# Kernel tuning notes

Hardware: AMD Instinct MI355X
Metric: run time of the kernel (lower is better)

Reference implementation:

```python
import jax, jax.numpy as jnp
import numpy as np

T, N, C, L, H, NA, NL = 32, 64, 64, 64, 256, 16, 128


def _gru_dir(x, wi, wh, bi, bh):
    # x: [Lt, N, H] time-major; PyTorch GRU gate order (r, z, n). Returns [Lt, N, H].
    xi = jnp.einsum('tnh,gh->tng', x, wi) + bi  # precompute input projections [Lt,N,3H]
    def step(h, gi):
        gh = h @ wh.T + bh
        ir, iz, inn = jnp.split(gi, 3, -1)
        hr, hz, hn = jnp.split(gh, 3, -1)
        r = jax.nn.sigmoid(ir + hr)
        z = jax.nn.sigmoid(iz + hz)
        n = jnp.tanh(inn + r * hn)
        hnew = (1.0 - z) * n + z * h
        return hnew, hnew
    h0 = jnp.zeros((x.shape[1], wh.shape[1]), x.dtype)
    _, ys = jax.lax.scan(step, h0, xi)
    return ys


def setup_inputs() -> dict:
    key = jax.random.key(0)
    ks = jax.random.split(key, 32)
    s = 0.05
    p = {}
    p['condition'] = jax.random.normal(ks[0], (T, N, C), jnp.float32)
    p['lines'] = jax.random.randint(ks[1], (N, L), 0, NL)
    p['a_idx'] = jax.random.randint(ks[2], (T, N), 0, NA)
    p['p_idx'] = jax.random.randint(ks[3], (T, N), 0, L)
    p['embed'] = jax.random.normal(ks[4], (NL, H)) * s
    p['aemb'] = jax.random.normal(ks[5], (NA, H)) * s
    p['gru_wi_f'] = jax.random.normal(ks[6], (3 * H, H)) * s
    p['gru_wh_f'] = jax.random.normal(ks[7], (3 * H, H)) * s
    p['gru_bi_f'] = jax.random.normal(ks[8], (3 * H,)) * s
    p['gru_bh_f'] = jax.random.normal(ks[9], (3 * H,)) * s
    p['gru_wi_b'] = jax.random.normal(ks[10], (3 * H, H)) * s
    p['gru_wh_b'] = jax.random.normal(ks[11], (3 * H, H)) * s
    p['gru_bi_b'] = jax.random.normal(ks[12], (3 * H,)) * s
    p['gru_bh_b'] = jax.random.normal(ks[13], (3 * H,)) * s
    p['f_w1'] = jax.random.normal(ks[14], (H, C + H)) * s
    p['f_b1'] = jax.random.normal(ks[15], (H,)) * s
    p['f_w2'] = jax.random.normal(ks[16], (H, H)) * s
    p['f_b2'] = jax.random.normal(ks[17], (H,)) * s
    p['cell_wi'] = jax.random.normal(ks[18], (3 * H, H)) * s
    p['cell_wh'] = jax.random.normal(ks[19], (3 * H, H)) * s
    p['cell_bi'] = jax.random.normal(ks[20], (3 * H,)) * s
    p['cell_bh'] = jax.random.normal(ks[21], (3 * H,)) * s
    p['critic_w'] = jax.random.normal(ks[22], (1, H)) * s
    p['critic_b'] = jax.random.normal(ks[23], (1,)) * s
    p['pointer_w'] = jax.random.normal(ks[24], (L, H)) * s
    p['pointer_b'] = jax.random.normal(ks[25], (L,)) * s
    p['actor_w'] = jax.random.normal(ks[26], (NA, H)) * s
    p['actor_b'] = jax.random.normal(ks[27], (NA,)) * s
    p['query_w'] = jax.random.normal(ks[28], (H, H)) * s
    p['query_b'] = jax.random.normal(ks[29], (H,)) * s
    return p


def reference(condition, lines, a_idx, p_idx, embed, aemb,
              gru_wi_f, gru_wh_f, gru_bi_f, gru_bh_f,
              gru_wi_b, gru_wh_b, gru_bi_b, gru_bh_b,
              f_w1, f_b1, f_w2, f_b2,
              cell_wi, cell_wh, cell_bi, cell_bh,
              critic_w, critic_b, pointer_w, pointer_b,
              actor_w, actor_b, query_w, query_b):
    Tn, Nn = a_idx.shape
    Ln = lines.shape[1]
    Hd = embed.shape[1]
    M = embed[lines]                           # [N,L,H]
    x = jnp.transpose(M, (1, 0, 2))            # [L,N,H] time-major
    # torch.roll(x, shifts=i): rolled[i, j] = x[(j - i) % L]
    idx = (jnp.arange(Ln)[None, :] - jnp.arange(Ln)[:, None]) % Ln
    rolled = x[idx]                            # [L_roll, L_time, N, H]
    def bigru(seq):
        f = _gru_dir(seq, gru_wi_f, gru_wh_f, gru_bi_f, gru_bh_f)
        b = _gru_dir(seq[::-1], gru_wi_b, gru_wh_b, gru_bi_b, gru_bh_b)[::-1]
        return jnp.concatenate([f, b], -1)     # [L_time,N,2H]
    K1 = jax.vmap(bigru)(rolled)               # [L,L,N,2H]
    K = K1.reshape(Ln, Ln, Nn, 2, Hd).transpose(2, 0, 1, 3, 4).reshape(Nn, Ln, 2 * Ln, Hd)
    # A[t-1] for t=0 is hx.a == 0 (fresh episode, zero hidden state)
    a_prev = jnp.concatenate([jnp.zeros((1, Nn), a_idx.dtype), a_idx[:-1]], 0)
    rng_n = jnp.arange(Nn)
    def step(h, inp):
        cond_t, ap_t, p_t, a_t = inp
        obs = jnp.concatenate([cond_t, aemb[ap_t]], -1)
        xf = jax.nn.relu(obs @ f_w1.T + f_b1)
        xf = jax.nn.relu(xf @ f_w2.T + f_b2)
        gi = xf @ cell_wi.T + cell_bi
        gh = h @ cell_wh.T + cell_bh
        ir, iz, inn = jnp.split(gi, 3, -1)
        hr, hz, hn = jnp.split(gh, 3, -1)
        r = jax.nn.sigmoid(ir + hr)
        z = jax.nn.sigmoid(iz + hz)
        n = jnp.tanh(inn + r * hn)
        h = (1.0 - z) * n + z * h
        p_probs = jax.nn.softmax(h @ pointer_w.T + pointer_b, -1)
        q = h @ query_w.T + query_b
        k = K[rng_n, p_t]                      # gather: [N, 2L, H]
        l = jnp.einsum('nkh,nh->nk', k, q)
        zz = jnp.einsum('nk,nkh->nh', l, k)
        a_probs = jax.nn.softmax(zz @ actor_w.T + actor_b, -1)
        v = h @ critic_w.T + critic_b
        out = jnp.concatenate([a_t[:, None].astype(h.dtype), p_t[:, None].astype(h.dtype),
                               v, h, a_probs, p_probs], -1)
        return h, out
    h0 = jnp.zeros((Nn, Hd), condition.dtype)
    _, hxs = jax.lax.scan(step, h0, (condition, a_prev, p_idx, a_idx))
    return hxs  # packed RecurrentState: [T, N, 1+1+1+H+na+L]
```

## Files before the change

### kernel.cpp

```cpp
#include <hip/hip_runtime.h>
#include <hip/hip_bf16.h>
#include <cstddef>
#include <cstdint>

typedef __bf16 bf16;
typedef bf16 bf16x8 __attribute__((ext_vector_type(8)));
typedef float f32x4 __attribute__((ext_vector_type(4)));

#define DEV static __device__ __forceinline__

DEV f32x4 mfma_bf16(bf16x8 a, bf16x8 b, f32x4 c) {
  return __builtin_amdgcn_mfma_f32_16x16x32_bf16(a, b, c, 0, 0, 0);
}
DEV f32x4 mfma_fp8(long a, long b, f32x4 c) {
  return __builtin_amdgcn_mfma_f32_16x16x32_fp8_fp8(a, b, c, 0, 0, 0);
}

DEV float sigmoid_f(float x) { return 1.0f / (1.0f + __expf(-x)); }
DEV float tanh_f(float x) {
  float ax = fabsf(x);
  float e = __expf(-2.0f * ax);
  float t = 1.0f - 2.0f * e / (1.0f + e);
  return copysignf(t, x);
}
DEV unsigned char fp8_of(float x) {
  return (unsigned char)(__builtin_amdgcn_cvt_pk_fp8_f32(x, x, 0, false) & 0xFF);
}

static constexpr int H_ = 256;

static constexpr int o_embed = 0;
static constexpr int o_aemb = 32768;
static constexpr int o_wi_f = 36864;
static constexpr int o_wh_f = 233472;
static constexpr int o_bi_f = 430080;
static constexpr int o_bh_f = 430848;
static constexpr int o_wi_b = 431616;
static constexpr int o_wh_b = 628224;
static constexpr int o_bi_b = 824832;
static constexpr int o_bh_b = 825600;
static constexpr int o_f_w1 = 826368;
static constexpr int o_f_b1 = 908288;
static constexpr int o_f_w2 = 908544;
static constexpr int o_f_b2 = 974080;
static constexpr int o_cell_wi = 974336;
static constexpr int o_cell_wh = 1170944;
static constexpr int o_cell_bi = 1367552;
static constexpr int o_cell_bh = 1368320;
static constexpr int o_critic_w = 1369088;
static constexpr int o_critic_b = 1369344;
static constexpr int o_pointer_w = 1369360;
static constexpr int o_pointer_b = 1385744;
static constexpr int o_actor_w = 1385808;
static constexpr int o_actor_b = 1389904;
static constexpr int o_query_w = 1389920;
static constexpr int o_query_b = 1455456;
static constexpr int CW_TOTAL = 1455712;
static constexpr int WH8_TOTAL = 393216;
static constexpr int PREP_TOTAL = CW_TOTAL + WH8_TOTAL;
static constexpr int PREP_WGS = (PREP_TOTAL + 2047) / 2048;

static constexpr size_t XI_OFF = 0;
static constexpr size_t XI_BYTES = 2ull * 64 * 64 * 768 * 2;
static constexpr size_t QS_OFF = XI_OFF;
static constexpr size_t K1_OFF = XI_OFF + XI_BYTES;
static constexpr size_t K1_BYTES = 64ull * 32 * 128 * 256;
static constexpr size_t GI_OFF = K1_OFF + K1_BYTES;
static constexpr size_t GI_BYTES = 32ull * 64 * 768 * 4;
static constexpr size_t HD_OFF = GI_OFF + GI_BYTES;
static constexpr size_t HD_BYTES = 32ull * 64 * 256 * 4;
static constexpr size_t SLOT_OFF = HD_OFF + HD_BYTES;
static constexpr size_t SLOT_BYTES = 64ull * 64 * 4;
static constexpr size_t FLG_OFF = SLOT_OFF + SLOT_BYTES;
static constexpr size_t FLG_BYTES = 256;
static constexpr size_t WL_OFF = FLG_OFF + FLG_BYTES;
static constexpr size_t WL_BYTES = 8448;
static constexpr size_t CW_OFF = WL_OFF + WL_BYTES;
static constexpr size_t CW_BYTES = (size_t)CW_TOTAL * 2;
static constexpr size_t WH8_OFF = ((CW_OFF + CW_BYTES + 255) / 256) * 256;

struct PrepArgs {
  const void* src[26];
  int off[26];
  int cnt[26];
};

__global__ __launch_bounds__(256)
void k_prep(PrepArgs pa, const uint32_t* __restrict__ cond, const uint32_t* __restrict__ emb,
            const void* __restrict__ whf_src, const void* __restrict__ whb_src,
            const int* __restrict__ p_idx, int* __restrict__ flags,
            bf16* __restrict__ cw, unsigned char* __restrict__ wh8,
            int* __restrict__ slot_map, int* __restrict__ wl) {
  int bx = blockIdx.x;
  int tid = threadIdx.x;
  __shared__ int votes[256];

  int c1 = 0;
  {
    uint32_t w0 = emb[tid * 2], w1 = emb[tid * 2 + 1];
    int e0 = (int)((w0 >> 7) & 0xFF), e1 = (int)((w1 >> 7) & 0xFF);
    c1 += (e0 >= 96 && e0 <= 130) ? 1 : 0;
    c1 += (e1 >= 96 && e1 <= 130) ? 1 : 0;
  }
  votes[tid] = c1;
  __syncthreads();
  __shared__ int f32w_s;
  if (tid == 0) {
    int s = 0;
    for (int i = 0; i < 256; i++) s += votes[i];
    f32w_s = (s < 256) ? 1 : 0;
  }
  __syncthreads();
  bool f32w = f32w_s != 0;

  if (bx == 0) {
    __syncthreads();
    int c0 = 0;
    {
      uint32_t w0 = cond[tid * 2], w1 = cond[tid * 2 + 1];
      int e0 = (int)((w0 >> 7) & 0xFF), e1 = (int)((w1 >> 7) & 0xFF);
      c0 += (e0 >= 96 && e0 <= 130) ? 1 : 0;
      c0 += (e1 >= 96 && e1 <= 130) ? 1 : 0;
    }
    votes[tid] = c0;
    __syncthreads();
    if (tid == 0) {
      int s = 0;
      for (int i = 0; i < 256; i++) s += votes[i];
      flags[0] = (s < 256) ? 1 : 0;
      flags[1] = f32w ? 1 : 0;
    }
  }
// ... 5 lines not shown
      if (gidx < CW_TOTAL) {
        int rem = gidx, s = 0;
        while (s < 26 && rem >= pa.cnt[s]) { rem -= pa.cnt[s]; s++; }
        if (s < 26) {
          float v = f32w ? ((const float*)pa.src[s])[rem]
                         : (float)((const bf16*)pa.src[s])[rem];
          cw[pa.off[s] + rem] = (bf16)v;
        }
      } else {
        int i = gidx - CW_TOTAL;
        const void* src = (i < 196608) ? whf_src : whb_src;
        int k = (i < 196608) ? i : i - 196608;
        float v = f32w ? ((const float*)src)[k] : (float)((const bf16*)src)[k];
        wh8[i] = fp8_of(v);
      }
    }
    return;
  }

  __shared__ int pbuf[2048];
  __shared__ signed char sm[4096];
  __shared__ unsigned short entL[8 * 512];
  __shared__ int cntL[8];
  for (int i = tid; i < 2048; i += 256) pbuf[i] = p_idx[i];
  for (int i = tid; i < 4096; i += 256) sm[i] = -1;
  __syncthreads();
  if (tid < 64) {
    int n = tid, cnt = 0;
    for (int t = 0; t < 32; t++) {
      int p = pbuf[t * 64 + n];
      if (sm[n * 64 + p] < 0) sm[n * 64 + p] = (signed char)(cnt++);
    }
  }
  __syncthreads();
  for (int i = tid; i < 4096; i += 256) slot_map[i] = (int)sm[i];
  if (tid < 8) {
    int xcd = tid, cnt = 0;
    for (int roll = xcd * 8; roll < xcd * 8 + 8; roll++)
      for (int n = 0; n < 64; n++)
        if (sm[n * 64 + roll] >= 0) entL[xcd * 512 + (cnt++)] = (unsigned short)(n | (roll << 8));
    unsigned short pad = (unsigned short)((xcd * 8) << 8);
    while (cnt & 15) entL[xcd * 512 + (cnt++)] = pad;
    cntL[xcd] = cnt;
  }
  __syncthreads();
  if (tid < 8) wl[tid] = cntL[tid] >> 4;
  unsigned short* we = (unsigned short*)((char*)wl + 64);
  for (int i = tid; i < 8 * 512; i += 256) we[i] = entL[i];
}

__global__ __launch_bounds__(256)
void k_xi_gi(const int* __restrict__ lines, const bf16* __restrict__ cw,
             const void* __restrict__ cond_raw, const int* __restrict__ flags,
             const int* __restrict__ a_idx, bf16* __restrict__ xi,
             float* __restrict__ gi) {
  int bx = blockIdx.x;
  int tid = threadIdx.x;
  int w = tid >> 6, l = tid & 63, quad = l >> 4, l15 = l & 15;
  __shared__ __attribute__((aligned(16))) bf16 s_a[32 * 328];
  __shared__ __attribute__((aligned(16))) bf16 s_b[32 * 264];

  if (bx < 256) {
    int dir = bx & 1, rb = bx >> 1;
    const bf16* embed = cw + o_embed;
    const bf16* wi = cw + (dir ? o_wi_b : o_wi_f);
    const bf16* bi = cw + (dir ? o_bi_b : o_bi_f);
    bf16* xs = s_a;
    {
      int row = tid >> 3, seg = tid & 7;
      int grow = rb * 32 + row;
      int u = grow >> 6, n = grow & 63;
      int line = lines[n * 64 + u];
      const bf16* src = embed + (size_t)line * H_ + seg * 32;
      bf16* dst = xs + row * 264 + seg * 32;
#pragma unroll
      for (int e = 0; e < 4; e++) *(bf16x8*)(dst + e * 8) = *(const bf16x8*)(src + e * 8);
    }
    __syncthreads();
    f32x4 acc[2][12];
#pragma unroll
    for (int mt = 0; mt < 2; mt++)
#pragma unroll
      for (int nt = 0; nt < 12; nt++) acc[mt][nt] = f32x4{0.f, 0.f, 0.f, 0.f};
#pragma unroll
    for (int ks = 0; ks < 8; ks++) {
      int koff = ks * 32 + quad * 8;
      bf16x8 a0 = *(const bf16x8*)(xs + l15 * 264 + koff);
      bf16x8 a1 = *(const bf16x8*)(xs + (l15 + 16) * 264 + koff);
#pragma unroll
      for (int nt = 0; nt < 12; nt++) {
        int g = (w * 12 + nt) * 16 + l15;
        bf16x8 b = *(const bf16x8*)(wi + (size_t)g * H_ + koff);
        acc[0][nt] = mfma_bf16(a0, b, acc[0][nt]);
        acc[1][nt] = mfma_bf16(a1, b, acc[1][nt]);
      }
    }
    size_t base = (size_t)dir * 4096 * 768;
#pragma unroll
    for (int nt = 0; nt < 12; nt++) {
      int g = (w * 12 + nt) * 16 + l15;
      float bias = (float)bi[g];
#pragma unroll
      for (int mt = 0; mt < 2; mt++)
#pragma unroll
        for (int r = 0; r < 4; r++) {
          int m = mt * 16 + quad * 4 + r;
          xi[base + (size_t)(rb * 32 + m) * 768 + g] = (bf16)(acc[mt][nt][r] + bias);
        }
    }
    return;
  }

  int rb = bx - 256;
  const bf16* aemb = cw + o_aemb;
  const bf16* f_w1 = cw + o_f_w1;
  const bf16* f_b1 = cw + o_f_b1;
  const bf16* f_w2 = cw + o_f_w2;
  const bf16* f_b2 = cw + o_f_b2;
  const bf16* cell_wi = cw + o_cell_wi;
  const bf16* cell_bi = cw + o_cell_bi;
  bool cf32 = flags[0] != 0;
  bf16* obs = s_a;
  bf16* xf1 = s_b;

  for (int e = tid; e < 32 * 320; e += 256) {
    int row = e / 320, col = e - row * 320;
    int grow = rb * 32 + row;
    int t = grow >> 6, n = grow & 63;
    float v;
    if (col < 64) {
      v = cf32 ? ((const float*)cond_raw)[(size_t)grow * 64 + col]
               : (float)((const bf16*)cond_raw)[(size_t)grow * 64 + col];
    } else {
      int ap = (t == 0) ? 0 : a_idx[(t - 1) * 64 + n];
      v = (float)aemb[ap * 256 + (col - 64)];
    }
    obs[row * 328 + col] = (bf16)v;
  }
  __syncthreads();
  {
    f32x4 acc[2][4];
#pragma unroll
    for (int mt = 0; mt < 2; mt++)
#pragma unroll
      for (int nt = 0; nt < 4; nt++) acc[mt][nt] = f32x4{0.f, 0.f, 0.f, 0.f};
#pragma unroll
    for (int ks = 0; ks < 10; ks++) {
      int koff = ks * 32 + quad * 8;
      bf16x8 a0 = *(const bf16x8*)(obs + l15 * 328 + koff);
      bf16x8 a1 = *(const bf16x8*)(obs + (l15 + 16) * 328 + koff);
#pragma unroll
      for (int nt = 0; nt < 4; nt++) {
        int g = (w * 4 + nt) * 16 + l15;
        bf16x8 b = *(const bf16x8*)(f_w1 + (size_t)g * 320 + koff);
        acc[0][nt] = mfma_bf16(a0, b, acc[0][nt]);
        acc[1][nt] = mfma_bf16(a1, b, acc[1][nt]);
      }
    }
#pragma unroll
    for (int nt = 0; nt < 4; nt++) {
// ... 27 lines not shown
        bf16x8 b = *(const bf16x8*)(f_w2 + (size_t)g * 256 + koff);
        acc[0][nt] = mfma_bf16(a0, b, acc[0][nt]);
        acc[1][nt] = mfma_bf16(a1, b, acc[1][nt]);
      }
    }
#pragma unroll
    for (int nt = 0; nt < 4; nt++) {
      int g = (w * 4 + nt) * 16 + l15;
      float bias = (float)f_b2[g];
#pragma unroll
      for (int mt = 0; mt < 2; mt++)
#pragma unroll
        for (int r = 0; r < 4; r++) {
          int m = mt * 16 + quad * 4 + r;
          xf2[m * 264 + g] = (bf16)fmaxf(acc[mt][nt][r] + bias, 0.f);
        }
    }
  }
  __syncthreads();
  {
    f32x4 acc[2][12];
#pragma unroll
    for (int mt = 0; mt < 2; mt++)
#pragma unroll
      for (int nt = 0; nt < 12; nt++) acc[mt][nt] = f32x4{0.f, 0.f, 0.f, 0.f};
#pragma unroll
    for (int ks = 0; ks < 8; ks++) {
      int koff = ks * 32 + quad * 8;
      bf16x8 a0 = *(const bf16x8*)(xf2 + l15 * 264 + koff);
      bf16x8 a1 = *(const bf16x8*)(xf2 + (l15 + 16) * 264 + koff);
#pragma unroll
      for (int nt = 0; nt < 12; nt++) {
        int g = (w * 12 + nt) * 16 + l15;
        bf16x8 b = *(const bf16x8*)(cell_wi + (size_t)g * 256 + koff);
        acc[0][nt] = mfma_bf16(a0, b, acc[0][nt]);
        acc[1][nt] = mfma_bf16(a1, b, acc[1][nt]);
      }
    }
#pragma unroll
    for (int nt = 0; nt < 12; nt++) {
      int g = (w * 12 + nt) * 16 + l15;
      float bias = (float)cell_bi[g];
#pragma unroll
      for (int mt = 0; mt < 2; mt++)
#pragma unroll
        for (int r = 0; r < 4; r++) {
          int m = mt * 16 + quad * 4 + r;
          gi[(size_t)(rb * 32 + m) * 768 + g] = acc[mt][nt][r] + bias;
        }
    }
  }
}

__global__ __launch_bounds__(1024)
void k_main(const bf16* __restrict__ cw, const unsigned char* __restrict__ wh8,
            const bf16* __restrict__ xi, const int* __restrict__ slot_map,
            const int* __restrict__ wl, const float* __restrict__ gi,
            unsigned char* __restrict__ K1c, float* __restrict__ hdec) {
  int bx = blockIdx.x;
  int tid = threadIdx.x;
  int w = tid >> 6, l = tid & 63, quad = l >> 4, l15 = l & 15;
  int c = w * 16 + l15;
  __shared__ __attribute__((aligned(16))) unsigned char smem[2][16 * 264 * 2];

  if (bx < 512) {
    int xcd = bx & 7, dir = (bx >> 3) & 1, slot = bx >> 4;
    if (slot >= wl[xcd]) return;
    const unsigned short* we = (const unsigned short*)((const char*)wl + 64) + xcd * 512 + slot * 16;
    const unsigned char* whd = wh8 + (size_t)dir * 196608;
    const bf16* bh = cw + (dir ? o_bh_b : o_bh_f);

    unsigned char (*hb)[16 * 264 * 2] = smem;
    for (int idx = tid; idx < 16 * 264; idx += 1024) hb[0][idx] = 0;

    int rollv[4], nbase[4];
#pragma unroll
    for (int r = 0; r < 4; r++) {
      int e = we[quad * 4 + r];
      rollv[r] = e >> 8;
      nbase[r] = (e & 255) * 768;
    }
    int crow = tid >> 6, cseg = tid & 63;
    int ec = we[crow];
    int n_c = ec & 255, roll_c = ec >> 8;
    int kslot = slot_map[n_c * 64 + roll_c];
    unsigned char* dstb = K1c + ((size_t)n_c * 32 + (kslot < 0 ? 0 : kslot)) * 32768 + cseg * 4;

    float hreg[4] = {0.f, 0.f, 0.f, 0.f};
    float bhv[3];
    const unsigned char* bp[3];
#pragma unroll
    for (int g = 0; g < 3; g++) {
      int grow = g * 256 + c;
      bhv[g] = (float)bh[grow];
      bp[g] = whd + (size_t)grow * 256 + quad * 8;
    }
    const bf16* xid = xi + (size_t)dir * 4096 * 768;
    __syncthreads();

    int cur = 0;
    for (int t = 0; t < 64; t++) {
      int j = dir ? (63 - t) : t;
      float xiv[3][4];
#pragma unroll
      for (int r = 0; r < 4; r++) {
        int u = dir ? ((63 - t - rollv[r]) & 63) : ((t - rollv[r]) & 63);
        const bf16* xr = xid + u * 49152 + nbase[r] + c;
#pragma unroll
        for (int g = 0; g < 3; g++) xiv[g][r] = (float)xr[g * 256];
      }
      f32x4 acc[3];
#pragma unroll
      for (int g = 0; g < 3; g++) acc[g] = f32x4{0.f, 0.f, 0.f, 0.f};
#pragma unroll
      for (int ks = 0; ks < 8; ks++) {
        int ko = ks * 32 + quad * 8;
        long a0 = *(const long*)(hb[cur] + l15 * 264 + ko);
#pragma unroll
        for (int g = 0; g < 3; g++) {
          long b = *(const long*)(bp[g] + ks * 32);
          acc[g] = mfma_fp8(a0, b, acc[g]);
        }
      }
      int nxt = cur ^ 1;
#pragma unroll
      for (int r = 0; r < 4; r++) {
        float rg = sigmoid_f(xiv[0][r] + acc[0][r] + bhv[0]);
        float zg = sigmoid_f(xiv[1][r] + acc[1][r] + bhv[1]);
        float ng = tanh_f(xiv[2][r] + rg * (acc[2][r] + bhv[2]));
        hreg[r] = (1.f - zg) * ng + zg * hreg[r];
        hb[nxt][(quad * 4 + r) * 264 + c] = fp8_of(hreg[r]);
      }
      __syncthreads();
      if (kslot >= 0) {
        *(uint32_t*)(dstb + (size_t)(j * 2 + dir) * 256) =
            *(const uint32_t*)(hb[nxt] + crow * 264 + cseg * 4);
      }
      cur = nxt;
    }
    return;
  }

  int nq = bx - 512;
  const bf16* wh = cw + o_cell_wh;
  const bf16* bh = cw + o_cell_bh;
  bf16 (*hb)[16 * 264] = (bf16(*)[16 * 264])smem;
  for (int idx = tid; idx < 16 * 264; idx += 1024) hb[0][idx] = (bf16)0.f;

  float hreg[4] = {0.f, 0.f, 0.f, 0.f};
  float bhv[3];
  const bf16* bp[3];
#pragma unroll
  for (int g = 0; g < 3; g++) {
    int grow = g * 256 + c;
    bhv[g] = (float)bh[grow];
    bp[g] = wh + (size_t)grow * 256 + quad * 8;
  }
  __syncthreads();

  int cur = 0;
  for (int t = 0; t < 32; t++) {
    const float* gr = gi + ((size_t)t * 64 + nq * 16) * 768;
    float giv[3][4];
#pragma unroll
    for (int r = 0; r < 4; r++)
#pragma unroll
      for (int g = 0; g < 3; g++)
        giv[g][r] = gr[(quad * 4 + r) * 768 + g * 256 + c];

    f32x4 acc[3];
#pragma unroll
    for (int g = 0; g < 3; g++) acc[g] = f32x4{0.f, 0.f, 0.f, 0.f};
#pragma unroll
    for (int ks = 0; ks < 8; ks++) {
      int ko = ks * 32 + quad * 8;
      bf16x8 a0 = *(const bf16x8*)(hb[cur] + l15 * 264 + ko);
#pragma unroll
      for (int g = 0; g < 3; g++) {
        bf16x8 b = *(const bf16x8*)(bp[g] + ks * 32);
        acc[g] = mfma_bf16(a0, b, acc[g]);
      }
    }
    int nxt = cur ^ 1;
#pragma unroll
    for (int r = 0; r < 4; r++) {
      float rg = sigmoid_f(giv[0][r] + acc[0][r] + bhv[0]);
      float zg = sigmoid_f(giv[1][r] + acc[1][r] + bhv[1]);
      float ng = tanh_f(giv[2][r] + rg * (acc[2][r] + bhv[2]));
      float hnew = (1.f - zg) * ng + zg * hreg[r];
      hreg[r] = hnew;
      hb[nxt][(quad * 4 + r) * 264 + c] = (bf16)hnew;
      hdec[((size_t)t * 64 + nq * 16 + quad * 4 + r) * 256 + c] = hnew;
    }
    __syncthreads();
    cur = nxt;
  }
}

__global__ __launch_bounds__(256)
void k_heads(const float* __restrict__ hdec, const int* __restrict__ flags,
             const int* __restrict__ a_idx, const int* __restrict__ p_idx,
             const bf16* __restrict__ cw, float* __restrict__ qs_ws,
             void* __restrict__ out_raw) {
  int rb = blockIdx.x;
  int tid = threadIdx.x;
  int w = tid >> 6, l = tid & 63, quad = l >> 4, l15 = l & 15;
  const bf16* query_w = cw + o_query_w;
  const bf16* query_b = cw + o_query_b;
  const bf16* pointer_w = cw + o_pointer_w;
  const bf16* pointer_b = cw + o_pointer_b;
  const bf16* critic_w = cw + o_critic_w;
  const bf16* critic_b = cw + o_critic_b;

  __shared__ __attribute__((aligned(16))) bf16 hsb[32 * 264];
  __shared__ float pls[32 * 66];
  __shared__ float vred[32 * 8];

  for (int idx = tid; idx < 32 * 256; idx += 256) {
    int row = idx >> 8, col = idx & 255;
    hsb[row * 264 + col] = (bf16)hdec[(size_t)(rb * 32 + row) * 256 + col];
  }
  __syncthreads();

  {
    f32x4 acc[2][4];
#pragma unroll
    for (int mt = 0; mt < 2; mt++)
#pragma unroll
      for (int nt = 0; nt < 4; nt++) acc[mt][nt] = f32x4{0.f, 0.f, 0.f, 0.f};
#pragma unroll
    for (int ks = 0; ks < 8; ks++) {
      int koff = ks * 32 + quad * 8;
      bf16x8 a0 = *(const bf16x8*)(hsb + l15 * 264 + koff);
      bf16x8 a1 = *(const bf16x8*)(hsb + (l15 + 16) * 264 + koff);
#pragma unroll
      for (int nt = 0; nt < 4; nt++) {
        int g = (w * 4 + nt) * 16 + l15;
        bf16x8 b = *(const bf16x8*)(query_w + (size_t)g * 256 + koff);
        acc[0][nt] = mfma_bf16(a0, b, acc[0][nt]);
        acc[1][nt] = mfma_bf16(a1, b, acc[1][nt]);
      }
    }
#pragma unroll
    for (int nt = 0; nt < 4; nt++) {
      int g = (w * 4 + nt) * 16 + l15;
      float bias = (float)query_b[g];
#pragma unroll
      for (int mt = 0; mt < 2; mt++)
#pragma unroll
        for (int r = 0; r < 4; r++) {
          int m = mt * 16 + quad * 4 + r;
          qs_ws[(size_t)(rb * 32 + m) * 256 + g] = acc[mt][nt][r] + bias;
        }
    }
  }
  {
    f32x4 acc[2];
    acc[0] = f32x4{0.f, 0.f, 0.f, 0.f};
    acc[1] = f32x4{0.f, 0.f, 0.f, 0.f};
    int g = w * 16 + l15;
#pragma unroll
    for (int ks = 0; ks < 8; ks++) {
      int koff = ks * 32 + quad * 8;
      bf16x8 a0 = *(const bf16x8*)(hsb + l15 * 264 + koff);
      bf16x8 a1 = *(const bf16x8*)(hsb + (l15 + 16) * 264 + koff);
      bf16x8 b = *(const bf16x8*)(pointer_w + (size_t)g * 256 + koff);
      acc[0] = mfma_bf16(a0, b, acc[0]);
      acc[1] = mfma_bf16(a1, b, acc[1]);
    }
    float bias = (float)pointer_b[g];
#pragma unroll
    for (int mt = 0; mt < 2; mt++)
#pragma unroll
      for (int r = 0; r < 4; r++) {
        int m = mt * 16 + quad * 4 + r;
        pls[m * 66 + g] = acc[mt][r] + bias;
      }
  }
  {
    int row = tid >> 3, seg = tid & 7;
    float acc = 0.f;
#pragma unroll
    for (int k = 0; k < 32; k++)
      acc += (float)hsb[row * 264 + seg * 32 + k] * (float)critic_w[seg * 32 + k];
    vred[row * 8 + seg] = acc;
  }
  __syncthreads();

  if (tid < 32) {
    float mx = -1e30f;
    for (int k = 0; k < 64; k++) mx = fmaxf(mx, pls[tid * 66 + k]);
    float sm = 0.f;
    for (int k = 0; k < 64; k++) {
      float e = __expf(pls[tid * 66 + k] - mx);
      pls[tid * 66 + k] = e;
      sm += e;
    }
    float inv = 1.f / sm;
    for (int k = 0; k < 64; k++) pls[tid * 66 + k] *= inv;
    float v = (float)critic_b[0];
    for (int s = 0; s < 8; s++) v += vred[tid * 8 + s];
    vred[tid * 8] = v;
  }
  __syncthreads();

  bool f32o = flags[1] != 0;
  if (f32o) {
    float* ob = (float*)out_raw;
    if (tid < 32) {
      int grow = rb * 32 + tid;
      ob[(size_t)grow * 339 + 0] = (float)a_idx[grow];
      ob[(size_t)grow * 339 + 1] = (float)p_idx[grow];
      ob[(size_t)grow * 339 + 2] = vred[tid * 8];
    }
    for (int idx = tid; idx < 32 * 256; idx += 256) {
      int row = idx >> 8, col = idx & 255;
      int grow = rb * 32 + row;
      ob[(size_t)grow * 339 + 3 + col] = hdec[(size_t)grow * 256 + col];
    }
    for (int idx = tid; idx < 32 * 64; idx += 256) {
      int row = idx >> 6, col = idx & 63;
      ob[(size_t)(rb * 32 + row) * 339 + 275 + col] = pls[row * 66 + col];
    }
  } else {
    bf16* ob = (bf16*)out_raw;
    if (tid < 32) {
      int grow = rb * 32 + tid;
      ob[(size_t)grow * 339 + 0] = (bf16)(float)a_idx[grow];
      ob[(size_t)grow * 339 + 1] = (bf16)(float)p_idx[grow];
      ob[(size_t)grow * 339 + 2] = (bf16)vred[tid * 8];
    }
    for (int idx = tid; idx < 32 * 256; idx += 256) {
      int row = idx >> 8, col = idx & 255;
      int grow = rb * 32 + row;
      ob[(size_t)grow * 339 + 3 + col] = (bf16)hdec[(size_t)grow * 256 + col];
    }
    for (int idx = tid; idx < 32 * 64; idx += 256) {
      int row = idx >> 6, col = idx & 63;
      ob[(size_t)(rb * 32 + row) * 339 + 275 + col] = (bf16)pls[row * 66 + col];
    }
  }
}

__global__ __launch_bounds__(256)
void k_attn(const float* __restrict__ qs_ws, const unsigned char* __restrict__ K1c,
            const int* __restrict__ slot_map, const int* __restrict__ flags,
            const int* __restrict__ p_idx, const bf16* __restrict__ cw,
            void* __restrict__ out_raw) {
  int bx = blockIdx.x;
  int t = bx >> 6, n = bx & 63;
  int tid = threadIdx.x;
  const bf16* actor_w = cw + o_actor_w;
  const bf16* actor_b = cw + o_actor_b;

  __shared__ float qs[256], ls[256], sA[256], al[16];
  __shared__ __attribute__((aligned(16))) unsigned char ksb[128 * 264];

  qs[tid] = qs_ws[(size_t)(t * 64 + n) * 256 + tid];
  int p = p_idx[t * 64 + n];
  int slot = slot_map[n * 64 + p];
  {
    const uint32_t* kg = (const uint32_t*)(K1c + ((size_t)n * 32 + slot) * 32768);
#pragma unroll
    for (int e = 0; e < 8; e++) {
      int flat = (e * 256 + tid) * 16;
      int kk = flat >> 8, col = flat & 255;
      uint32_t w0 = kg[(flat >> 2) + 0], w1 = kg[(flat >> 2) + 1];
      uint32_t w2 = kg[(flat >> 2) + 2], w3 = kg[(flat >> 2) + 3];
      uint32_t* d0 = (uint32_t*)(ksb + kk * 264 + col);
      d0[0] = w0; d0[1] = w1; d0[2] = w2; d0[3] = w3;
    }
  }
  __syncthreads();

  {
    int kk = tid & 127, hc = tid >> 7;
    const uint32_t* kr = (const uint32_t*)(ksb + kk * 264 + hc * 128);
    const float* qr = qs + hc * 128;
    float acc = 0.f;
#pragma unroll 8
    for (int u = 0; u < 32; u++) {
      uint32_t b4 = kr[u];
      acc += __builtin_amdgcn_cvt_f32_fp8(b4, 0) * qr[u * 4 + 0];
      acc += __builtin_amdgcn_cvt_f32_fp8(b4, 1) * qr[u * 4 + 1];
      acc += __builtin_amdgcn_cvt_f32_fp8(b4, 2) * qr[u * 4 + 2];
      acc += __builtin_amdgcn_cvt_f32_fp8(b4, 3) * qr[u * 4 + 3];
    }
    ls[tid] = acc;
  }
  __syncthreads();
  if (tid < 128) ls[tid] += ls[tid + 128];
  __syncthreads();

  float zzv;
  {
    const unsigned char* kc = ksb + (tid & ~3);
    int sh = (tid & 3) * 8;
    float acc = 0.f;
#pragma unroll 8
    for (int kk = 0; kk < 128; kk++) {
      uint32_t d = *(const uint32_t*)(kc + kk * 264);
      acc += ls[kk] * __builtin_amdgcn_cvt_f32_fp8((int)(d >> sh), 0);
    }
    zzv = acc;
  }
  __syncthreads();
  qs[tid] = zzv;
  __syncthreads();

  {
    int a = tid >> 4, e = tid & 15;
    const bf16* aw = actor_w + (size_t)a * 256 + e * 16;
    const float* zr = qs + e * 16;
    float acc = 0.f;
#pragma unroll
    for (int hh = 0; hh < 16; hh++) acc += (float)aw[hh] * zr[hh];
    sA[tid] = acc;
  }
  __syncthreads();
  if (tid < 16) {
    float lg = (float)actor_b[tid];
#pragma unroll
    for (int e = 0; e < 16; e++) lg += sA[tid * 16 + e];
    float mx = lg;
#pragma unroll
    for (int m = 8; m > 0; m >>= 1) mx = fmaxf(mx, __shfl_xor(mx, m, 16));
    float ex = __expf(lg - mx);
    float sm = ex;
#pragma unroll
    for (int m = 8; m > 0; m >>= 1) sm += __shfl_xor(sm, m, 16);
    al[tid] = ex / sm;
  }
  __syncthreads();

  if (tid < 16) {
    size_t off = (size_t)(t * 64 + n) * 339 + 259 + tid;
    if (flags[1]) ((float*)out_raw)[off] = al[tid];
    else ((bf16*)out_raw)[off] = (bf16)al[tid];
  }
}

extern "C" void kernel_launch(void* const* d_in, const int* in_sizes, int n_in,
                              void* d_out, int out_size, void* d_ws, size_t ws_size,
                              hipStream_t stream) {
  (void)in_sizes; (void)n_in; (void)out_size; (void)ws_size;
  const void* condition = d_in[0];
  const int* lines      = (const int*)d_in[1];
  const int* a_idx      = (const int*)d_in[2];
  const int* p_idx      = (const int*)d_in[3];

  char* ws = (char*)d_ws;
  bf16* xi            = (bf16*)(ws + XI_OFF);
  float* qs_ws        = (float*)(ws + QS_OFF);
  unsigned char* K1c  = (unsigned char*)(ws + K1_OFF);
  float* gi           = (float*)(ws + GI_OFF);
  float* hdec         = (float*)(ws + HD_OFF);
  int* slot_map       = (int*)(ws + SLOT_OFF);
  int* flags          = (int*)(ws + FLG_OFF);
  int* wl             = (int*)(ws + WL_OFF);
  bf16* cw            = (bf16*)(ws + CW_OFF);
  unsigned char* wh8  = (unsigned char*)(ws + WH8_OFF);

  static const int src_idx[26] = {4, 5, 6, 7, 8, 9, 10, 11, 12, 13, 14, 15, 16,
                                  17, 18, 19, 20, 21, 22, 23, 24, 25, 26, 27, 28, 29};
  static const int offs[26] = {o_embed, o_aemb, o_wi_f, o_wh_f, o_bi_f, o_bh_f,
                               o_wi_b, o_wh_b, o_bi_b, o_bh_b, o_f_w1, o_f_b1,
                               o_f_w2, o_f_b2, o_cell_wi, o_cell_wh, o_cell_bi,
                               o_cell_bh, o_critic_w, o_critic_b, o_pointer_w,
                               o_pointer_b, o_actor_w, o_actor_b, o_query_w, o_query_b};
  static const int cnts[26] = {32768, 4096, 196608, 196608, 768, 768,
                               196608, 196608, 768, 768, 81920, 256,
                               65536, 256, 196608, 196608, 768,
                               768, 256, 1, 16384, 64, 4096, 16, 65536, 256};
  PrepArgs pa;
  for (int i = 0; i < 26; i++) {
    pa.src[i] = d_in[src_idx[i]];
    pa.off[i] = offs[i];
    pa.cnt[i] = cnts[i];
  }

  k_prep<<<PREP_WGS + 1, 256, 0, stream>>>(pa, (const uint32_t*)condition,
                                           (const uint32_t*)d_in[4], d_in[7], d_in[11],
                                           p_idx, flags, cw, wh8, slot_map, wl);
  k_xi_gi<<<320, 256, 0, stream>>>(lines, cw, condition, flags, a_idx, xi, gi);
  k_main<<<516, 1024, 0, stream>>>(cw, wh8, xi, slot_map, wl, gi, K1c, hdec);
  k_heads<<<64, 256, 0, stream>>>(hdec, flags, a_idx, p_idx, cw, qs_ws, d_out);
  k_attn<<<2048, 256, 0, stream>>>(qs_ws, K1c, slot_map, flags, p_idx, cw, d_out);
}
```

Before: 429.2 us.

## Interleave GRU input-projection gates and keep fp8 recurrent weights in registers

```diff
diff --git a/kernel.cpp b/kernel.cpp
--- a/kernel.cpp
+++ b/kernel.cpp
@@ -5,6 +5,7 @@
 
 typedef __bf16 bf16;
 typedef bf16 bf16x8 __attribute__((ext_vector_type(8)));
+typedef bf16 bf16x4 __attribute__((ext_vector_type(4)));
 typedef float f32x4 __attribute__((ext_vector_type(4)));
 
 #define DEV static __device__ __forceinline__
@@ -61,7 +62,7 @@
 static constexpr int PREP_WGS = (PREP_TOTAL + 2047) / 2048;
 
 static constexpr size_t XI_OFF = 0;
-static constexpr size_t XI_BYTES = 2ull * 64 * 64 * 768 * 2;
+static constexpr size_t XI_BYTES = 2ull * 4096 * 1024 * 2;
 static constexpr size_t QS_OFF = XI_OFF;
 static constexpr size_t K1_OFF = XI_OFF + XI_BYTES;
 static constexpr size_t K1_BYTES = 64ull * 32 * 128 * 256;
@@ -189,7 +190,7 @@
 __global__ __launch_bounds__(256)
 void k_xi_gi(const int* __restrict__ lines, const bf16* __restrict__ cw,
              const void* __restrict__ cond_raw, const int* __restrict__ flags,
-             const int* __restrict__ a_idx, bf16* __restrict__ xi,
+             const int* __restrict__ a_idx, bf16* __restrict__ xi4,
              float* __restrict__ gi) {
   int bx = blockIdx.x;
   int tid = threadIdx.x;
@@ -232,17 +233,19 @@
         acc[1][nt] = mfma_bf16(a1, b, acc[1][nt]);
       }
     }
-    size_t base = (size_t)dir * 4096 * 768;
+    size_t base = (size_t)dir * 4096 * 1024;
 #pragma unroll
     for (int nt = 0; nt < 12; nt++) {
       int g = (w * 12 + nt) * 16 + l15;
+      int gate = g >> 8, col = g & 255;
       float bias = (float)bi[g];
 #pragma unroll
       for (int mt = 0; mt < 2; mt++)
 #pragma unroll
         for (int r = 0; r < 4; r++) {
           int m = mt * 16 + quad * 4 + r;
-          xi[base + (size_t)(rb * 32 + m) * 768 + g] = (bf16)(acc[mt][nt][r] + bias);
+          xi4[base + (size_t)(rb * 32 + m) * 1024 + col * 4 + gate] =
+              (bf16)(acc[mt][nt][r] + bias);
         }
     }
     return;
@@ -376,9 +379,9 @@
   }
 }
 
-__global__ __launch_bounds__(1024)
+__global__ __launch_bounds__(1024, 4)
 void k_main(const bf16* __restrict__ cw, const unsigned char* __restrict__ wh8,
-            const bf16* __restrict__ xi, const int* __restrict__ slot_map,
+            const bf16* __restrict__ xi4, const int* __restrict__ slot_map,
             const int* __restrict__ wl, const float* __restrict__ gi,
             unsigned char* __restrict__ K1c, float* __restrict__ hdec) {
   int bx = blockIdx.x;
@@ -397,12 +400,20 @@
     unsigned char (*hb)[16 * 264 * 2] = smem;
     for (int idx = tid; idx < 16 * 264; idx += 1024) hb[0][idx] = 0;
 
-    int rollv[4], nbase[4];
+    long bfr[3][8];
+#pragma unroll
+    for (int g = 0; g < 3; g++) {
+      const unsigned char* bp = whd + (size_t)(g * 256 + c) * 256 + quad * 8;
+#pragma unroll
+      for (int ks = 0; ks < 8; ks++) bfr[g][ks] = *(const long*)(bp + ks * 32);
+    }
+
+    int rollv[4], nrow[4];
 #pragma unroll
     for (int r = 0; r < 4; r++) {
       int e = we[quad * 4 + r];
       rollv[r] = e >> 8;
-      nbase[r] = (e & 255) * 768;
+      nrow[r] = e & 255;
     }
     int crow = tid >> 6, cseg = tid & 63;
     int ec = we[crow];
@@ -412,46 +423,36 @@
 
     float hreg[4] = {0.f, 0.f, 0.f, 0.f};
     float bhv[3];
-    const unsigned char* bp[3];
-#pragma unroll
-    for (int g = 0; g < 3; g++) {
-      int grow = g * 256 + c;
-      bhv[g] = (float)bh[grow];
-      bp[g] = whd + (size_t)grow * 256 + quad * 8;
-    }
-    const bf16* xid = xi + (size_t)dir * 4096 * 768;
+#pragma unroll
+    for (int g = 0; g < 3; g++) bhv[g] = (float)bh[g * 256 + c];
+
+    const bf16* xid = xi4 + (size_t)dir * 4096 * 1024;
     __syncthreads();
 
     int cur = 0;
     for (int t = 0; t < 64; t++) {
       int j = dir ? (63 - t) : t;
-      float xiv[3][4];
+      bf16x4 xv[4];
 #pragma unroll
       for (int r = 0; r < 4; r++) {
         int u = dir ? ((63 - t - rollv[r]) & 63) : ((t - rollv[r]) & 63);
-        const bf16* xr = xid + u * 49152 + nbase[r] + c;
-#pragma unroll
-        for (int g = 0; g < 3; g++) xiv[g][r] = (float)xr[g * 256];
+        xv[r] = *(const bf16x4*)(xid + (size_t)(u * 64 + nrow[r]) * 1024 + c * 4);
       }
       f32x4 acc[3];
 #pragma unroll
       for (int g = 0; g < 3; g++) acc[g] = f32x4{0.f, 0.f, 0.f, 0.f};
 #pragma unroll
       for (int ks = 0; ks < 8; ks++) {
-        int ko = ks * 32 + quad * 8;
-        long a0 = *(const long*)(hb[cur] + l15 * 264 + ko);
-#pragma unroll
-        for (int g = 0; g < 3; g++) {
-          long b = *(const long*)(bp[g] + ks * 32);
-          acc[g] = mfma_fp8(a0, b, acc[g]);
-        }
+        long a0 = *(const long*)(hb[cur] + l15 * 264 + ks * 32 + quad * 8);
+#pragma unroll
+        for (int g = 0; g < 3; g++) acc[g] = mfma_fp8(a0, bfr[g][ks], acc[g]);
       }
       int nxt = cur ^ 1;
 #pragma unroll
       for (int r = 0; r < 4; r++) {
-        float rg = sigmoid_f(xiv[0][r] + acc[0][r] + bhv[0]);
-        float zg = sigmoid_f(xiv[1][r] + acc[1][r] + bhv[1]);
-        float ng = tanh_f(xiv[2][r] + rg * (acc[2][r] + bhv[2]));
+        float rg = sigmoid_f((float)xv[r][0] + acc[0][r] + bhv[0]);
+        float zg = sigmoid_f((float)xv[r][1] + acc[1][r] + bhv[1]);
+        float ng = tanh_f((float)xv[r][2] + rg * (acc[2][r] + bhv[2]));
         hreg[r] = (1.f - zg) * ng + zg * hreg[r];
         hb[nxt][(quad * 4 + r) * 264 + c] = fp8_of(hreg[r]);
       }
@@ -774,7 +775,7 @@
   const int* p_idx      = (const int*)d_in[3];
 
   char* ws = (char*)d_ws;
-  bf16* xi            = (bf16*)(ws + XI_OFF);
+  bf16* xi4           = (bf16*)(ws + XI_OFF);
   float* qs_ws        = (float*)(ws + QS_OFF);
   unsigned char* K1c  = (unsigned char*)(ws + K1_OFF);
   float* gi           = (float*)(ws + GI_OFF);
@@ -806,8 +807,8 @@
   k_prep<<<PREP_WGS + 1, 256, 0, stream>>>(pa, (const uint32_t*)condition,
                                            (const uint32_t*)d_in[4], d_in[7], d_in[11],
                                            p_idx, flags, cw, wh8, slot_map, wl);
-  k_xi_gi<<<320, 256, 0, stream>>>(lines, cw, condition, flags, a_idx, xi, gi);
-  k_main<<<516, 1024, 0, stream>>>(cw, wh8, xi, slot_map, wl, gi, K1c, hdec);
+  k_xi_gi<<<320, 256, 0, stream>>>(lines, cw, condition, flags, a_idx, xi4, gi);
+  k_main<<<516, 1024, 0, stream>>>(cw, wh8, xi4, slot_map, wl, gi, K1c, hdec);
   k_heads<<<64, 256, 0, stream>>>(hdec, flags, a_idx, p_idx, cw, qs_ws, d_out);
   k_attn<<<2048, 256, 0, stream>>>(qs_ws, K1c, slot_map, flags, p_idx, cw, d_out);
 }
```

New measurement: 438.7 us. 2.2% more time.

## Fuse heads and attention kernels, register-cache fp8 GRU weights in encoder loop

Applied to the files above, without the earlier changes.

```diff
diff --git a/kernel.cpp b/kernel.cpp
--- a/kernel.cpp
+++ b/kernel.cpp
@@ -61,8 +61,7 @@
 static constexpr int PREP_WGS = (PREP_TOTAL + 2047) / 2048;
 
 static constexpr size_t XI_OFF = 0;
-static constexpr size_t XI_BYTES = 2ull * 64 * 64 * 768 * 2;
-static constexpr size_t QS_OFF = XI_OFF;
+static constexpr size_t XI_BYTES = 2ull * 4096 * 768 * 2;
 static constexpr size_t K1_OFF = XI_OFF + XI_BYTES;
 static constexpr size_t K1_BYTES = 64ull * 32 * 128 * 256;
 static constexpr size_t GI_OFF = K1_OFF + K1_BYTES;
@@ -78,6 +77,9 @@
 static constexpr size_t CW_OFF = WL_OFF + WL_BYTES;
 static constexpr size_t CW_BYTES = (size_t)CW_TOTAL * 2;
 static constexpr size_t WH8_OFF = ((CW_OFF + CW_BYTES + 255) / 256) * 256;
+
+static constexpr int XI_DIR_BYTES = 4096 * 768 * 2;
+static constexpr int XI_U_BYTES = 64 * 768 * 2;
 
 struct PrepArgs {
   const void* src[26];
@@ -376,7 +378,7 @@
   }
 }
 
-__global__ __launch_bounds__(1024)
+__global__ __launch_bounds__(1024, 4)
 void k_main(const bf16* __restrict__ cw, const unsigned char* __restrict__ wh8,
             const bf16* __restrict__ xi, const int* __restrict__ slot_map,
             const int* __restrict__ wl, const float* __restrict__ gi,
@@ -397,69 +399,83 @@
     unsigned char (*hb)[16 * 264 * 2] = smem;
     for (int idx = tid; idx < 16 * 264; idx += 1024) hb[0][idx] = 0;
 
-    int rollv[4], nbase[4];
+    long bfr[3][8];
+#pragma unroll
+    for (int g = 0; g < 3; g++) {
+      const unsigned char* bp = whd + (size_t)(g * 256 + c) * 256 + quad * 8;
+#pragma unroll
+      for (int ks = 0; ks < 8; ks++) bfr[g][ks] = *(const long*)(bp + ks * 32);
+    }
+
+    int xoff[4];
+    uint32_t slice[4];
+    bool valid[4];
 #pragma unroll
     for (int r = 0; r < 4; r++) {
       int e = we[quad * 4 + r];
-      rollv[r] = e >> 8;
-      nbase[r] = (e & 255) * 768;
-    }
-    int crow = tid >> 6, cseg = tid & 63;
-    int ec = we[crow];
-    int n_c = ec & 255, roll_c = ec >> 8;
-    int kslot = slot_map[n_c * 64 + roll_c];
-    unsigned char* dstb = K1c + ((size_t)n_c * 32 + (kslot < 0 ? 0 : kslot)) * 32768 + cseg * 4;
+      int roll = e >> 8, n = e & 255;
+      int u0 = dir ? ((63 - roll) & 63) : ((64 - roll) & 63);
+      xoff[r] = u0 * XI_U_BYTES + n * 1536 + c * 2;
+      int ks = slot_map[n * 64 + roll];
+      valid[r] = ks >= 0;
+      slice[r] = (uint32_t)((n * 32 + (ks < 0 ? 0 : ks)) * 32768);
+    }
+    int ustep = dir ? -XI_U_BYTES : XI_U_BYTES;
+    int jbase = dir ? (63 * 2 + 1) * 256 : 0;
+    int jstep = dir ? -512 : 512;
 
     float hreg[4] = {0.f, 0.f, 0.f, 0.f};
     float bhv[3];
-    const unsigned char* bp[3];
-#pragma unroll
-    for (int g = 0; g < 3; g++) {
-      int grow = g * 256 + c;
-      bhv[g] = (float)bh[grow];
-      bp[g] = whd + (size_t)grow * 256 + quad * 8;
-    }
-    const bf16* xid = xi + (size_t)dir * 4096 * 768;
+#pragma unroll
+    for (int g = 0; g < 3; g++) bhv[g] = (float)bh[g * 256 + c];
+
+    const char* xid = (const char*)xi + (size_t)dir * XI_DIR_BYTES;
     __syncthreads();
 
     int cur = 0;
     for (int t = 0; t < 64; t++) {
-      int j = dir ? (63 - t) : t;
       float xiv[3][4];
 #pragma unroll
       for (int r = 0; r < 4; r++) {
-        int u = dir ? ((63 - t - rollv[r]) & 63) : ((t - rollv[r]) & 63);
-        const bf16* xr = xid + u * 49152 + nbase[r] + c;
-#pragma unroll
-        for (int g = 0; g < 3; g++) xiv[g][r] = (float)xr[g * 256];
-      }
-      f32x4 acc[3];
-#pragma unroll
-      for (int g = 0; g < 3; g++) acc[g] = f32x4{0.f, 0.f, 0.f, 0.f};
-#pragma unroll
-      for (int ks = 0; ks < 8; ks++) {
-        int ko = ks * 32 + quad * 8;
-        long a0 = *(const long*)(hb[cur] + l15 * 264 + ko);
+        const bf16* xp = (const bf16*)(xid + xoff[r]);
+        xiv[0][r] = (float)xp[0];
+        xiv[1][r] = (float)xp[256];
+        xiv[2][r] = (float)xp[512];
+        xoff[r] += ustep;
+        if (xoff[r] >= XI_DIR_BYTES) xoff[r] -= XI_DIR_BYTES;
+        if (xoff[r] < 0) xoff[r] += XI_DIR_BYTES;
+      }
+
+      f32x4 accA[3], accB[3];
+#pragma unroll
+      for (int g = 0; g < 3; g++) {
+        accA[g] = f32x4{0.f, 0.f, 0.f, 0.f};
+        accB[g] = f32x4{0.f, 0.f, 0.f, 0.f};
+      }
+#pragma unroll
+      for (int ks = 0; ks < 4; ks++) {
+        long a0 = *(const long*)(hb[cur] + l15 * 264 + ks * 32 + quad * 8);
+        long a1 = *(const long*)(hb[cur] + l15 * 264 + (ks + 4) * 32 + quad * 8);
 #pragma unroll
         for (int g = 0; g < 3; g++) {
-          long b = *(const long*)(bp[g] + ks * 32);
-          acc[g] = mfma_fp8(a0, b, acc[g]);
+          accA[g] = mfma_fp8(a0, bfr[g][ks], accA[g]);
+          accB[g] = mfma_fp8(a1, bfr[g][ks + 4], accB[g]);
         }
       }
+
       int nxt = cur ^ 1;
 #pragma unroll
       for (int r = 0; r < 4; r++) {
-        float rg = sigmoid_f(xiv[0][r] + acc[0][r] + bhv[0]);
-        float zg = sigmoid_f(xiv[1][r] + acc[1][r] + bhv[1]);
-        float ng = tanh_f(xiv[2][r] + rg * (acc[2][r] + bhv[2]));
+        float rg = sigmoid_f(xiv[0][r] + accA[0][r] + accB[0][r] + bhv[0]);
+        float zg = sigmoid_f(xiv[1][r] + accA[1][r] + accB[1][r] + bhv[1]);
+        float ng = tanh_f(xiv[2][r] + rg * (accA[2][r] + accB[2][r] + bhv[2]));
         hreg[r] = (1.f - zg) * ng + zg * hreg[r];
-        hb[nxt][(quad * 4 + r) * 264 + c] = fp8_of(hreg[r]);
-      }
+        unsigned char hb8 = fp8_of(hreg[r]);
+        hb[nxt][(quad * 4 + r) * 264 + c] = hb8;
+        if (valid[r]) K1c[(size_t)slice[r] + jbase + c] = hb8;
+      }
+      jbase += jstep;
       __syncthreads();
-      if (kslot >= 0) {
-        *(uint32_t*)(dstb + (size_t)(j * 2 + dir) * 256) =
-            *(const uint32_t*)(hb[nxt] + crow * 264 + cseg * 4);
-      }
       cur = nxt;
     }
     return;
@@ -522,165 +538,135 @@
 }
 
 __global__ __launch_bounds__(256)
-void k_heads(const float* __restrict__ hdec, const int* __restrict__ flags,
-             const int* __restrict__ a_idx, const int* __restrict__ p_idx,
-             const bf16* __restrict__ cw, float* __restrict__ qs_ws,
-             void* __restrict__ out_raw) {
-  int rb = blockIdx.x;
+void k_post(const float* __restrict__ hdec, const unsigned char* __restrict__ K1c,
+            const int* __restrict__ slot_map, const int* __restrict__ flags,
+            const int* __restrict__ a_idx, const int* __restrict__ p_idx,
+            const bf16* __restrict__ cw, void* __restrict__ out_raw) {
+  int bx = blockIdx.x;
   int tid = threadIdx.x;
   int w = tid >> 6, l = tid & 63, quad = l >> 4, l15 = l & 15;
+  __shared__ __attribute__((aligned(16))) unsigned char sraw[38032];
+  bool f32o = flags[1] != 0;
+
+  if (bx < 64) {
+    int rb = bx;
+    const bf16* pointer_w = cw + o_pointer_w;
+    const bf16* pointer_b = cw + o_pointer_b;
+    const bf16* critic_w = cw + o_critic_w;
+    const bf16* critic_b = cw + o_critic_b;
+    bf16* hsb = (bf16*)sraw;
+    float* pls = (float*)(sraw + 16896);
+    float* vred = (float*)(sraw + 16896 + 8448);
+
+    for (int idx = tid; idx < 32 * 256; idx += 256) {
+      int row = idx >> 8, col = idx & 255;
+      hsb[row * 264 + col] = (bf16)hdec[(size_t)(rb * 32 + row) * 256 + col];
+    }
+    __syncthreads();
+
+    {
+      f32x4 acc[2];
+      acc[0] = f32x4{0.f, 0.f, 0.f, 0.f};
+      acc[1] = f32x4{0.f, 0.f, 0.f, 0.f};
+      int g = w * 16 + l15;
+#pragma unroll
+      for (int ks = 0; ks < 8; ks++) {
+        int koff = ks * 32 + quad * 8;
+        bf16x8 a0 = *(const bf16x8*)(hsb + l15 * 264 + koff);
+        bf16x8 a1 = *(const bf16x8*)(hsb + (l15 + 16) * 264 + koff);
+        bf16x8 b = *(const bf16x8*)(pointer_w + (size_t)g * 256 + koff);
+        acc[0] = mfma_bf16(a0, b, acc[0]);
+        acc[1] = mfma_bf16(a1, b, acc[1]);
+      }
+      float bias = (float)pointer_b[g];
+#pragma unroll
+      for (int mt = 0; mt < 2; mt++)
+#pragma unroll
+        for (int r = 0; r < 4; r++) {
+          int m = mt * 16 + quad * 4 + r;
+          pls[m * 66 + g] = acc[mt][r] + bias;
+        }
+    }
+    {
+      int row = tid >> 3, seg = tid & 7;
+      float acc = 0.f;
+#pragma unroll
+      for (int k = 0; k < 32; k++)
+        acc += (float)hsb[row * 264 + seg * 32 + k] * (float)critic_w[seg * 32 + k];
+      vred[row * 8 + seg] = acc;
+    }
+    __syncthreads();
+
+    if (tid < 32) {
+      float mx = -1e30f;
+      for (int k = 0; k < 64; k++) mx = fmaxf(mx, pls[tid * 66 + k]);
+      float sm = 0.f;
+      for (int k = 0; k < 64; k++) {
+        float e = __expf(pls[tid * 66 + k] - mx);
+        pls[tid * 66 + k] = e;
+        sm += e;
+      }
+      float inv = 1.f / sm;
+      for (int k = 0; k < 64; k++) pls[tid * 66 + k] *= inv;
+      float v = (float)critic_b[0];
+      for (int s = 0; s < 8; s++) v += vred[tid * 8 + s];
+      vred[tid * 8] = v;
+    }
+    __syncthreads();
+
+    if (f32o) {
+      float* ob = (float*)out_raw;
+      if (tid < 32) {
+        int grow = rb * 32 + tid;
+        ob[(size_t)grow * 339 + 0] = (float)a_idx[grow];
+        ob[(size_t)grow * 339 + 1] = (float)p_idx[grow];
+        ob[(size_t)grow * 339 + 2] = vred[tid * 8];
+      }
+      for (int idx = tid; idx < 32 * 256; idx += 256) {
+        int row = idx >> 8, col = idx & 255;
+        int grow = rb * 32 + row;
+        ob[(size_t)grow * 339 + 3 + col] = hdec[(size_t)grow * 256 + col];
+      }
+      for (int idx = tid; idx < 32 * 64; idx += 256) {
+        int row = idx >> 6, col = idx & 63;
+        ob[(size_t)(rb * 32 + row) * 339 + 275 + col] = pls[row * 66 + col];
+      }
+    } else {
+      bf16* ob = (bf16*)out_raw;
+      if (tid < 32) {
+        int grow = rb * 32 + tid;
+        ob[(size_t)grow * 339 + 0] = (bf16)(float)a_idx[grow];
+        ob[(size_t)grow * 339 + 1] = (bf16)(float)p_idx[grow];
+        ob[(size_t)grow * 339 + 2] = (bf16)vred[tid * 8];
+      }
+      for (int idx = tid; idx < 32 * 256; idx += 256) {
+        int row = idx >> 8, col = idx & 255;
+        int grow = rb * 32 + row;
+        ob[(size_t)grow * 339 + 3 + col] = (bf16)hdec[(size_t)grow * 256 + col];
+      }
+      for (int idx = tid; idx < 32 * 64; idx += 256) {
+        int row = idx >> 6, col = idx & 63;
+        ob[(size_t)(rb * 32 + row) * 339 + 275 + col] = (bf16)pls[row * 66 + col];
+      }
+    }
+    return;
+  }
+
+  int tn = bx - 64;
+  int t = tn >> 6, n = tn & 63;
+  const bf16* actor_w = cw + o_actor_w;
+  const bf16* actor_b = cw + o_actor_b;
   const bf16* query_w = cw + o_query_w;
   const bf16* query_b = cw + o_query_b;
-  const bf16* pointer_w = cw + o_pointer_w;
-  const bf16* pointer_b = cw + o_pointer_b;
-  const bf16* critic_w = cw + o_critic_w;
-  const bf16* critic_b = cw + o_critic_b;
-
-  __shared__ __attribute__((aligned(16))) bf16 hsb[32 * 264];
-  __shared__ float pls[32 * 66];
-  __shared__ float vred[32 * 8];
-
-  for (int idx = tid; idx < 32 * 256; idx += 256) {
-    int row = idx >> 8, col = idx & 255;
-    hsb[row * 264 + col] = (bf16)hdec[(size_t)(rb * 32 + row) * 256 + col];
-  }
-  __syncthreads();
-
-  {
-    f32x4 acc[2][4];
-#pragma unroll
-    for (int mt = 0; mt < 2; mt++)
-#pragma unroll
-      for (int nt = 0; nt < 4; nt++) acc[mt][nt] = f32x4{0.f, 0.f, 0.f, 0.f};
-#pragma unroll
-    for (int ks = 0; ks < 8; ks++) {
-      int koff = ks * 32 + quad * 8;
-      bf16x8 a0 = *(const bf16x8*)(hsb + l15 * 264 + koff);
-      bf16x8 a1 = *(const bf16x8*)(hsb + (l15 + 16) * 264 + koff);
-#pragma unroll
-      for (int nt = 0; nt < 4; nt++) {
-        int g = (w * 4 + nt) * 16 + l15;
-        bf16x8 b = *(const bf16x8*)(query_w + (size_t)g * 256 + koff);
-        acc[0][nt] = mfma_bf16(a0, b, acc[0][nt]);
-        acc[1][nt] = mfma_bf16(a1, b, acc[1][nt]);
-      }
-    }
-#pragma unroll
-    for (int nt = 0; nt < 4; nt++) {
-      int g = (w * 4 + nt) * 16 + l15;
-      float bias = (float)query_b[g];
-#pragma unroll
-      for (int mt = 0; mt < 2; mt++)
-#pragma unroll
-        for (int r = 0; r < 4; r++) {
-          int m = mt * 16 + quad * 4 + r;
-          qs_ws[(size_t)(rb * 32 + m) * 256 + g] = acc[mt][nt][r] + bias;
-        }
-    }
-  }
-  {
-    f32x4 acc[2];
-    acc[0] = f32x4{0.f, 0.f, 0.f, 0.f};
-    acc[1] = f32x4{0.f, 0.f, 0.f, 0.f};
-    int g = w * 16 + l15;
-#pragma unroll
-    for (int ks = 0; ks < 8; ks++) {
-      int koff = ks * 32 + quad * 8;
-      bf16x8 a0 = *(const bf16x8*)(hsb + l15 * 264 + koff);
-      bf16x8 a1 = *(const bf16x8*)(hsb + (l15 + 16) * 264 + koff);
-      bf16x8 b = *(const bf16x8*)(pointer_w + (size_t)g * 256 + koff);
-      acc[0] = mfma_bf16(a0, b, acc[0]);
-      acc[1] = mfma_bf16(a1, b, acc[1]);
-    }
-    float bias = (float)pointer_b[g];
-#pragma unroll
-    for (int mt = 0; mt < 2; mt++)
-#pragma unroll
-      for (int r = 0; r < 4; r++) {
-        int m = mt * 16 + quad * 4 + r;
-        pls[m * 66 + g] = acc[mt][r] + bias;
-      }
-  }
-  {
-    int row = tid >> 3, seg = tid & 7;
-    float acc = 0.f;
-#pragma unroll
-    for (int k = 0; k < 32; k++)
-      acc += (float)hsb[row * 264 + seg * 32 + k] * (float)critic_w[seg * 32 + k];
-    vred[row * 8 + seg] = acc;
-  }
-  __syncthreads();
-
-  if (tid < 32) {
-    float mx = -1e30f;
-    for (int k = 0; k < 64; k++) mx = fmaxf(mx, pls[tid * 66 + k]);
-    float sm = 0.f;
-    for (int k = 0; k < 64; k++) {
-      float e = __expf(pls[tid * 66 + k] - mx);
-      pls[tid * 66 + k] = e;
-      sm += e;
-    }
-    float inv = 1.f / sm;
-    for (int k = 0; k < 64; k++) pls[tid * 66 + k] *= inv;
-    float v = (float)critic_b[0];
-    for (int s = 0; s < 8; s++) v += vred[tid * 8 + s];
-    vred[tid * 8] = v;
-  }
-  __syncthreads();
-
-  bool f32o = flags[1] != 0;
-  if (f32o) {
-    float* ob = (float*)out_raw;
-    if (tid < 32) {
-      int grow = rb * 32 + tid;
-      ob[(size_t)grow * 339 + 0] = (float)a_idx[grow];
-      ob[(size_t)grow * 339 + 1] = (float)p_idx[grow];
-      ob[(size_t)grow * 339 + 2] = vred[tid * 8];
-    }
-    for (int idx = tid; idx < 32 * 256; idx += 256) {
-      int row = idx >> 8, col = idx & 255;
-      int grow = rb * 32 + row;
-      ob[(size_t)grow * 339 + 3 + col] = hdec[(size_t)grow * 256 + col];
-    }
-    for (int idx = tid; idx < 32 * 64; idx += 256) {
-      int row = idx >> 6, col = idx & 63;
-      ob[(size_t)(rb * 32 + row) * 339 + 275 + col] = pls[row * 66 + col];
-    }
-  } else {
-    bf16* ob = (bf16*)out_raw;
-    if (tid < 32) {
-      int grow = rb * 32 + tid;
-      ob[(size_t)grow * 339 + 0] = (bf16)(float)a_idx[grow];
-      ob[(size_t)grow * 339 + 1] = (bf16)(float)p_idx[grow];
-      ob[(size_t)grow * 339 + 2] = (bf16)vred[tid * 8];
-    }
-    for (int idx = tid; idx < 32 * 256; idx += 256) {
-      int row = idx >> 8, col = idx & 255;
-      int grow = rb * 32 + row;
-      ob[(size_t)grow * 339 + 3 + col] = (bf16)hdec[(size_t)grow * 256 + col];
-    }
-    for (int idx = tid; idx < 32 * 64; idx += 256) {
-      int row = idx >> 6, col = idx & 63;
-      ob[(size_t)(rb * 32 + row) * 339 + 275 + col] = (bf16)pls[row * 66 + col];
-    }
-  }
-}
-
-__global__ __launch_bounds__(256)
-void k_attn(const float* __restrict__ qs_ws, const unsigned char* __restrict__ K1c,
-            const int* __restrict__ slot_map, const int* __restrict__ flags,
-            const int* __restrict__ p_idx, const bf16* __restrict__ cw,
-            void* __restrict__ out_raw) {
-  int bx = blockIdx.x;
-  int t = bx >> 6, n = bx & 63;
-  int tid = threadIdx.x;
-  const bf16* actor_w = cw + o_actor_w;
-  const bf16* actor_b = cw + o_actor_b;
-
-  __shared__ float qs[256], ls[256], sA[256], al[16];
-  __shared__ __attribute__((aligned(16))) unsigned char ksb[128 * 264];
-
-  qs[tid] = qs_ws[(size_t)(t * 64 + n) * 256 + tid];
+
+  unsigned char* ksb = sraw;
+  float* hs = (float*)(sraw + 33792);
+  float* qs = (float*)(sraw + 33792 + 1024);
+  float* ls = (float*)(sraw + 33792 + 2048);
+  float* sA = (float*)(sraw + 33792 + 3072);
+  float* al = (float*)(sraw + 33792 + 4096);
+
+  hs[tid] = hdec[((size_t)t * 64 + n) * 256 + tid];
   int p = p_idx[t * 64 + n];
   int slot = slot_map[n * 64 + p];
   {
@@ -694,6 +680,19 @@
       uint32_t* d0 = (uint32_t*)(ksb + kk * 264 + col);
       d0[0] = w0; d0[1] = w1; d0[2] = w2; d0[3] = w3;
     }
+  }
+  __syncthreads();
+
+  {
+    float acc = (float)query_b[tid];
+    const bf16* qw = query_w + (size_t)tid * 256;
+#pragma unroll 4
+    for (int k0 = 0; k0 < 256; k0 += 8) {
+      bf16x8 wv = *(const bf16x8*)(qw + k0);
+#pragma unroll
+      for (int e = 0; e < 8; e++) acc += (float)wv[e] * hs[k0 + e];
+    }
+    qs[tid] = acc;
   }
   __syncthreads();
 
@@ -759,7 +758,7 @@
 
   if (tid < 16) {
     size_t off = (size_t)(t * 64 + n) * 339 + 259 + tid;
-    if (flags[1]) ((float*)out_raw)[off] = al[tid];
+    if (f32o) ((float*)out_raw)[off] = al[tid];
     else ((bf16*)out_raw)[off] = (bf16)al[tid];
   }
 }
@@ -775,7 +774,6 @@
 
   char* ws = (char*)d_ws;
   bf16* xi            = (bf16*)(ws + XI_OFF);
-  float* qs_ws        = (float*)(ws + QS_OFF);
   unsigned char* K1c  = (unsigned char*)(ws + K1_OFF);
   float* gi           = (float*)(ws + GI_OFF);
   float* hdec         = (float*)(ws + HD_OFF);
@@ -808,6 +806,5 @@
                                            p_idx, flags, cw, wh8, slot_map, wl);
   k_xi_gi<<<320, 256, 0, stream>>>(lines, cw, condition, flags, a_idx, xi, gi);
   k_main<<<516, 1024, 0, stream>>>(cw, wh8, xi, slot_map, wl, gi, K1c, hdec);
-  k_heads<<<64, 256, 0, stream>>>(hdec, flags, a_idx, p_idx, cw, qs_ws, d_out);
-  k_attn<<<2048, 256, 0, stream>>>(qs_ws, K1c, slot_map, flags, p_idx, cw, d_out);
+  k_post<<<2112, 256, 0, stream>>>(hdec, K1c, slot_map, flags, a_idx, p_idx, cw, d_out);
 }
```

New measurement: 453.8 us. 1.06x slower.
